# Kernel optimization log

Measured on AMD Instinct MI355X. Metric: run time of the kernel, lower is better.

Reference implementation:

```python
import jax, jax.numpy as jnp
import numpy as np
from jax import lax

B, S, I = 256, 2048, 128
H, K, O, M = 32, 64, 256, 3


def setup_inputs() -> dict:
    key = jax.random.key(0)
    ks = jax.random.split(key, 11)
    sc_i = 1.0 / np.sqrt(I)
    sc_h = 1.0 / np.sqrt(H)
    return {
        "inputs": jax.random.normal(ks[0], (B, S, I), dtype=jnp.float32),
        "W_ih": jax.random.uniform(ks[1], (3 * H, I), jnp.float32, -sc_h, sc_h),
        "W_hh": jax.random.uniform(ks[2], (3 * H, H), jnp.float32, -sc_h, sc_h),
        "b_ih": jax.random.uniform(ks[3], (3 * H,), jnp.float32, -sc_h, sc_h),
        "b_hh": jax.random.uniform(ks[4], (3 * H,), jnp.float32, -sc_h, sc_h),
        "Wk": jax.random.uniform(ks[5], (K, H), jnp.float32, -sc_h, sc_h),
        "bk": jax.random.uniform(ks[6], (K,), jnp.float32, -sc_h, sc_h),
        "Wq": jax.random.uniform(ks[7], (K, H), jnp.float32, -sc_h, sc_h),
        "bq": jax.random.uniform(ks[8], (K,), jnp.float32, -sc_h, sc_h),
        "Wv": jax.random.uniform(ks[9], (O, H), jnp.float32, -sc_h, sc_h),
        "bv": jax.random.uniform(ks[10], (O,), jnp.float32, -sc_h, sc_h),
    }


def _gru_cell(x, h, W_ih, W_hh, b_ih, b_hh):
    # torch.nn.GRUCell math
    gi = x @ W_ih.T + b_ih  # (B, 3H)
    gh = h @ W_hh.T + b_hh  # (B, 3H)
    i_r, i_z, i_n = jnp.split(gi, 3, axis=-1)
    h_r, h_z, h_n = jnp.split(gh, 3, axis=-1)
    r = jax.nn.sigmoid(i_r + h_r)
    z = jax.nn.sigmoid(i_z + h_z)
    n = jnp.tanh(i_n + r * h_n)
    return (1.0 - z) * n + z * h


def reference(inputs, W_ih, W_hh, b_ih, b_hh, Wk, bk, Wq, bq, Wv, bv):
    Bb, Ss, _ = inputs.shape
    dt = inputs.dtype
    NEG = jnp.asarray(-1e30, dt)

    def step(carry, xt):
        x_t, t = xt
        h, keys, values = carry
        h = _gru_cell(x_t, h, W_ih, W_hh, b_ih, b_hh)
        # read (counter == t at read time, capped at M via valid mask)
        q = h @ Wq.T + bq                              # (B, K)
        valid = jnp.arange(M) < t                      # (M,)
        scores = jnp.einsum('bk,bmk->bm', q, keys)
        scores = jnp.where(valid[None, :], scores, NEG)
        w = jax.nn.softmax(scores, axis=-1)
        retrieved = jnp.einsum('bm,bmo->bo', w, values)
        retrieved = retrieved * (t > 0).astype(dt)     # counter==0 -> zeros
        # write (only first M steps)
        key_t = h @ Wk.T + bk                          # (B, K)
        val_t = h @ Wv.T + bv                          # (B, O)
        oh = jax.nn.one_hot(t, M, dtype=dt) * (t < M).astype(dt)  # (M,)
        keys = keys + oh[None, :, None] * key_t[:, None, :]
        values = values + oh[None, :, None] * val_t[:, None, :]
        return (h, keys, values), (retrieved, h)

    init = (jnp.zeros((Bb, H), dt), jnp.zeros((Bb, M, K), dt), jnp.zeros((Bb, M, O), dt))
    xs = jnp.swapaxes(inputs, 0, 1)                    # (S, B, I)
    ts = jnp.arange(Ss)
    _, (outs, hids) = lax.scan(step, init, (xs, ts))
    outputs = jnp.swapaxes(outs, 0, 1)                 # (B, S, O)
    hiddens = lax.stop_gradient(jnp.swapaxes(hids, 0, 1))  # detached in torch
    return outputs, hiddens
```

## Files before the change

### kernel.cpp

```cpp
#include <hip/hip_runtime.h>
#include <cstddef>

#define Bq   256
#define Sq   2048
#define Iq   128
#define Hq   32
#define THq  96
#define Kq   64
#define Oq   256
#define Mq   3

#define OUT_HID_OFF 134217728ull
#define GI_BSTRIDE  524288ull
#define GI_OFF      327680ull

__global__ __launch_bounds__(256) void gi_gemm_kernel(
    const float* __restrict__ x, const float* __restrict__ Wih,
    const float* __restrict__ bih, float* __restrict__ gi_base)
{
    __shared__ float Wl[THq * Iq];
    const int tid = threadIdx.x;

    {
        const float4* Wg4 = (const float4*)Wih;
        float4* Wl4 = (float4*)Wl;
        #pragma unroll
        for (int i = 0; i < 12; ++i)
            Wl4[tid + 256 * i] = Wg4[tid + 256 * i];
    }
    __syncthreads();

    const int r = blockIdx.x * 256 + tid;
    const int b = r >> 11;
    const int s = r & 2047;

    const float4* xg = (const float4*)(x + (size_t)r * Iq);
    float4 xv[32];
    #pragma unroll
    for (int i = 0; i < 32; ++i) xv[i] = xg[i];

    float* out = gi_base + (size_t)b * GI_BSTRIDE + GI_OFF + (size_t)s * THq;

    #pragma unroll
    for (int half = 0; half < 2; ++half) {
        float acc[48];
        #pragma unroll
        for (int j = 0; j < 48; ++j) {
            const int row = half * 48 + j;
            const float4* w4 = (const float4*)(Wl + row * Iq);
            float p0 = bih[row], p1 = 0.f, p2 = 0.f, p3 = 0.f;
            #pragma unroll
            for (int i = 0; i < 32; ++i) {
                float4 w = w4[i];
                float4 xx = xv[i];
                p0 = fmaf(xx.x, w.x, p0);
                p1 = fmaf(xx.y, w.y, p1);
                p2 = fmaf(xx.z, w.z, p2);
                p3 = fmaf(xx.w, w.w, p3);
            }
            acc[j] = (p0 + p1) + (p2 + p3);
        }
        float4* o4 = (float4*)(out + half * 48);
        #pragma unroll
        for (int j4 = 0; j4 < 12; ++j4)
            o4[j4] = make_float4(acc[4*j4+0], acc[4*j4+1], acc[4*j4+2], acc[4*j4+3]);
    }
}

__device__ __forceinline__ float sigmoid_f(float x) {
    return 1.f / (1.f + __expf(-x));
}
__device__ __forceinline__ float tanh_f(float x) {
    x = fminf(fmaxf(x, -30.f), 30.f);
    float e = __expf(-2.f * x);
    return (1.f - e) / (1.f + e);
}

__global__ __launch_bounds__(128) void scan_kernel(
    const float* __restrict__ Whh, const float* __restrict__ bhh,
    const float* __restrict__ Wk,  const float* __restrict__ bk,
    const float* __restrict__ Wq,  const float* __restrict__ bq,
    const float* __restrict__ Wv,  const float* __restrict__ bv,
    float* __restrict__ dout)
{
    const int tid = threadIdx.x;
    const int b = blockIdx.x;

    __shared__ __align__(16) float hbuf[2][Hq];
    __shared__ __align__(16) float keysS[Mq][Kq];
    __shared__ __align__(16) float valsS[Mq][Oq];

    if (tid < Hq) { hbuf[0][tid] = 0.f; hbuf[1][tid] = 0.f; }
    for (int i = tid; i < Mq * Kq; i += 128) ((float*)keysS)[i] = 0.f;
    for (int i = tid; i < Mq * Oq; i += 128) ((float*)valsS)[i] = 0.f;

    const float* gi_row = dout + (size_t)b * GI_BSTRIDE + GI_OFF;
    float* out_o = dout + (size_t)b * GI_BSTRIDE;
    float* out_h = dout + OUT_HID_OFF + (size_t)b * (Sq * Hq);

    if (tid < 64) {
        const int l = tid;
        const bool lo = (l < Hq);
        float wa[Hq], wb[Hq];
        #pragma unroll
        for (int k = 0; k < Hq; ++k) wa[k] = Whh[l * Hq + k];
        #pragma unroll
        for (int k = 0; k < Hq; ++k) wb[k] = lo ? Whh[(64 + l) * Hq + k] : 0.f;
        const float ba = bhh[l];
        const float bb = lo ? bhh[64 + l] : 0.f;
        float h_old = 0.f;

        const int PF = 4;
        float ga[4], gb[4];
        #pragma unroll
        for (int d = 0; d < PF; ++d) {
            ga[d] = gi_row[(size_t)d * THq + l];
            gb[d] = lo ? gi_row[(size_t)d * THq + 64 + l] : 0.f;
        }

        for (int t = 0; t <= Sq; ++t) {
            __syncthreads();
            if (t < Sq) {
                const float gia = ga[0];
                const float gib = gb[0];
                #pragma unroll
                for (int d = 0; d < PF - 1; ++d) { ga[d] = ga[d+1]; gb[d] = gb[d+1]; }
                const int tt = t + PF;
                if (tt < Sq) {
                    ga[PF-1] = gi_row[(size_t)tt * THq + l];
                    gb[PF-1] = lo ? gi_row[(size_t)tt * THq + 64 + l] : 0.f;
                } else { ga[PF-1] = 0.f; gb[PF-1] = 0.f; }

                const float4* h4 = (const float4*)hbuf[(t + 1) & 1];
                float gha = ba, ghb = bb;
                #pragma unroll
                for (int kk = 0; kk < 8; ++kk) {
                    float4 hv = h4[kk];
                    gha = fmaf(hv.x, wa[4*kk+0], gha);
                    gha = fmaf(hv.y, wa[4*kk+1], gha);
                    gha = fmaf(hv.z, wa[4*kk+2], gha);
                    gha = fmaf(hv.w, wa[4*kk+3], gha);
                    ghb = fmaf(hv.x, wb[4*kk+0], ghb);
                    ghb = fmaf(hv.y, wb[4*kk+1], ghb);
                    ghb = fmaf(hv.z, wb[4*kk+2], ghb);
                    ghb = fmaf(hv.w, wb[4*kk+3], ghb);
                }
                const float xa = gia + gha;
                const float xz = __shfl(xa, l + 32, 64);
                if (lo) {
                    const float r = sigmoid_f(xa);
                    const float z = sigmoid_f(xz);
                    const float n = tanh_f(gib + r * ghb);
                    const float hn = (1.f - z) * n + z * h_old;
                    h_old = hn;
                    hbuf[t & 1][l] = hn;
                    out_h[(size_t)t * Hq + l] = hn;
                }
            }
        }
    } else {
        const int k = tid - 64;
        float wqr[Hq], wkr[Hq];
        #pragma unroll
        for (int kk = 0; kk < Hq; ++kk) wqr[kk] = Wq[k * Hq + kk];
        #pragma unroll
        for (int kk = 0; kk < Hq; ++kk) wkr[kk] = Wk[k * Hq + kk];
        const float bqk = bq[k];
        const float bkk = bk[k];

        for (int t = 0; t <= Sq; ++t) {
            __syncthreads();
            if (t >= 1) {
                const int tp = t - 1;
                const float4* h4 = (const float4*)hbuf[tp & 1];
                float4 hr[8];
                #pragma unroll
                for (int kk = 0; kk < 8; ++kk) hr[kk] = h4[kk];

                float q = bqk;
                #pragma unroll
                for (int kk = 0; kk < 8; ++kk) {
                    q = fmaf(hr[kk].x, wqr[4*kk+0], q);
                    q = fmaf(hr[kk].y, wqr[4*kk+1], q);
                    q = fmaf(hr[kk].z, wqr[4*kk+2], q);
                    q = fmaf(hr[kk].w, wqr[4*kk+3], q);
                }
                float s0 = q * keysS[0][k];
                float s1 = q * keysS[1][k];
                float s2 = q * keysS[2][k];
                #pragma unroll
                for (int off = 1; off < 64; off <<= 1) {
                    s0 += __shfl_xor(s0, off, 64);
                    s1 += __shfl_xor(s1, off, 64);
                    s2 += __shfl_xor(s2, off, 64);
                }
                const int v = tp < Mq ? tp : Mq;
                float w0 = 0.f, w1 = 0.f, w2 = 0.f;
                if (v > 0) {
                    float mx = s0;
                    if (v > 1) mx = fmaxf(mx, s1);
                    if (v > 2) mx = fmaxf(mx, s2);
                    const float e0 = __expf(s0 - mx);
                    const float e1 = (v > 1) ? __expf(s1 - mx) : 0.f;
                    const float e2 = (v > 2) ? __expf(s2 - mx) : 0.f;
                    const float inv = 1.f / (e0 + e1 + e2);
                    w0 = e0 * inv; w1 = e1 * inv; w2 = e2 * inv;
                }
                const float4 a0 = ((const float4*)valsS[0])[k];
                const float4 a1 = ((const float4*)valsS[1])[k];
                const float4 a2 = ((const float4*)valsS[2])[k];
                float4 acc;
                acc.x = w0*a0.x + w1*a1.x + w2*a2.x;
                acc.y = w0*a0.y + w1*a1.y + w2*a2.y;
                acc.z = w0*a0.z + w1*a1.z + w2*a2.z;
                acc.w = w0*a0.w + w1*a1.w + w2*a2.w;
                ((float4*)(out_o + (size_t)tp * Oq))[k] = acc;

                if (tp < Mq) {
                    float kv = bkk;
                    #pragma unroll
                    for (int kk = 0; kk < 8; ++kk) {
                        kv = fmaf(hr[kk].x, wkr[4*kk+0], kv);
                        kv = fmaf(hr[kk].y, wkr[4*kk+1], kv);
                        kv = fmaf(hr[kk].z, wkr[4*kk+2], kv);
                        kv = fmaf(hr[kk].w, wkr[4*kk+3], kv);
                    }
                    keysS[tp][k] = kv;
                    #pragma unroll
                    for (int j = 0; j < 4; ++j) {
                        const int o = 4 * k + j;
                        const float* wvr = Wv + o * Hq;
                        float vv = bv[o];
                        #pragma unroll
                        for (int kk = 0; kk < 8; ++kk) {
                            vv = fmaf(hr[kk].x, wvr[4*kk+0], vv);
                            vv = fmaf(hr[kk].y, wvr[4*kk+1], vv);
                            vv = fmaf(hr[kk].z, wvr[4*kk+2], vv);
                            vv = fmaf(hr[kk].w, wvr[4*kk+3], vv);
                        }
                        valsS[tp][o] = vv;
                    }
                }
            }
        }
    }
}

extern "C" void kernel_launch(void* const* d_in, const int* in_sizes, int n_in,
                              void* d_out, int out_size, void* d_ws, size_t ws_size,
                              hipStream_t stream) {
    const float* inputs = (const float*)d_in[0];
    const float* W_ih   = (const float*)d_in[1];
    const float* W_hh   = (const float*)d_in[2];
    const float* b_ih   = (const float*)d_in[3];
    const float* b_hh   = (const float*)d_in[4];
    const float* Wk     = (const float*)d_in[5];
    const float* bk     = (const float*)d_in[6];
    const float* Wq     = (const float*)d_in[7];
    const float* bq     = (const float*)d_in[8];
    const float* Wv     = (const float*)d_in[9];
    const float* bv     = (const float*)d_in[10];
    float* out = (float*)d_out;

    gi_gemm_kernel<<<(Bq * Sq) / 256, 256, 0, stream>>>(inputs, W_ih, b_ih, out);
    scan_kernel<<<Bq, 128, 0, stream>>>(W_hh, b_hh, Wk, bk, Wq, bq, Wv, bv, out);
}
```

Baseline: 2.410 ms.

## Fold query projection into precomputed key scores and tighten scan step latency

For each memory slot, the read path now precomputes A_m = Wq^T·key_m and the constant bq·key_m once, at write time. Each step's score then becomes a 32-wide dot product with h, which removes the per-step query projection and the 64-lane shuffle reductions from the serial critical path. The scan also uses a lighter LDS-only barrier, switches to hardware reciprocals in sigmoid, tanh and softmax, and moves the hidden-state stores to the idle read wavefront. Separately, the input GEMM accumulates all 96 outputs over four K-chunks with a two-blocks-per-CU launch bound, which raises register pressure. The reciprocal-based math and the reordered dot products slightly change floating-point rounding.

```diff
diff --git a/kernel.cpp b/kernel.cpp
--- a/kernel.cpp
+++ b/kernel.cpp
@@ -14,11 +14,12 @@
 #define GI_BSTRIDE  524288ull
 #define GI_OFF      327680ull
 
-__global__ __launch_bounds__(256) void gi_gemm_kernel(
+__global__ __launch_bounds__(256, 2) void gi_gemm_kernel(
     const float* __restrict__ x, const float* __restrict__ Wih,
     const float* __restrict__ bih, float* __restrict__ gi_base)
 {
-    __shared__ float Wl[THq * Iq];
+    __shared__ __align__(16) float Wl[THq * Iq];
+    __shared__ __align__(16) float Bl[THq];
     const int tid = threadIdx.x;
 
     {
@@ -27,31 +28,35 @@
         #pragma unroll
         for (int i = 0; i < 12; ++i)
             Wl4[tid + 256 * i] = Wg4[tid + 256 * i];
+        if (tid < THq) Bl[tid] = bih[tid];
     }
     __syncthreads();
 
     const int r = blockIdx.x * 256 + tid;
     const int b = r >> 11;
     const int s = r & 2047;
-
     const float4* xg = (const float4*)(x + (size_t)r * Iq);
-    float4 xv[32];
+
+    float acc[THq];
     #pragma unroll
-    for (int i = 0; i < 32; ++i) xv[i] = xg[i];
-
-    float* out = gi_base + (size_t)b * GI_BSTRIDE + GI_OFF + (size_t)s * THq;
-
-    #pragma unroll
-    for (int half = 0; half < 2; ++half) {
-        float acc[48];
-        #pragma unroll
-        for (int j = 0; j < 48; ++j) {
-            const int row = half * 48 + j;
-            const float4* w4 = (const float4*)(Wl + row * Iq);
-            float p0 = bih[row], p1 = 0.f, p2 = 0.f, p3 = 0.f;
+    for (int j4 = 0; j4 < 24; ++j4) {
+        float4 bv = ((const float4*)Bl)[j4];
+        acc[4*j4+0] = bv.x; acc[4*j4+1] = bv.y;
+        acc[4*j4+2] = bv.z; acc[4*j4+3] = bv.w;
+    }
+
+    #pragma unroll 1
+    for (int c = 0; c < 4; ++c) {
+        float4 xv[8];
+        #pragma unroll
+        for (int i = 0; i < 8; ++i) xv[i] = xg[c * 8 + i];
+        #pragma unroll
+        for (int j = 0; j < THq; ++j) {
+            const float4* w4 = (const float4*)(Wl + j * Iq) + c * 8;
+            float p0 = acc[j], p1 = 0.f, p2 = 0.f, p3 = 0.f;
             #pragma unroll
-            for (int i = 0; i < 32; ++i) {
-                float4 w = w4[i];
+            for (int i = 0; i < 8; ++i) {
+                float4 w  = w4[i];
                 float4 xx = xv[i];
                 p0 = fmaf(xx.x, w.x, p0);
                 p1 = fmaf(xx.y, w.y, p1);
@@ -60,20 +65,29 @@
             }
             acc[j] = (p0 + p1) + (p2 + p3);
         }
-        float4* o4 = (float4*)(out + half * 48);
-        #pragma unroll
-        for (int j4 = 0; j4 < 12; ++j4)
-            o4[j4] = make_float4(acc[4*j4+0], acc[4*j4+1], acc[4*j4+2], acc[4*j4+3]);
-    }
+    }
+
+    float* outp = gi_base + (size_t)b * GI_BSTRIDE + GI_OFF + (size_t)s * THq;
+    float4* o4 = (float4*)outp;
+    #pragma unroll
+    for (int j4 = 0; j4 < 24; ++j4)
+        o4[j4] = make_float4(acc[4*j4+0], acc[4*j4+1], acc[4*j4+2], acc[4*j4+3]);
+}
+
+__device__ __forceinline__ void lds_barrier() {
+    __builtin_amdgcn_sched_barrier(0);
+    asm volatile("s_waitcnt lgkmcnt(0)" ::: "memory");
+    __builtin_amdgcn_s_barrier();
+    __builtin_amdgcn_sched_barrier(0);
 }
 
 __device__ __forceinline__ float sigmoid_f(float x) {
-    return 1.f / (1.f + __expf(-x));
+    return __builtin_amdgcn_rcpf(1.f + __expf(-x));
 }
 __device__ __forceinline__ float tanh_f(float x) {
     x = fminf(fmaxf(x, -30.f), 30.f);
     float e = __expf(-2.f * x);
-    return (1.f - e) / (1.f + e);
+    return fmaf(2.f, __builtin_amdgcn_rcpf(1.f + e), -1.f);
 }
 
 __global__ __launch_bounds__(128) void scan_kernel(
@@ -89,10 +103,12 @@
     __shared__ __align__(16) float hbuf[2][Hq];
     __shared__ __align__(16) float keysS[Mq][Kq];
     __shared__ __align__(16) float valsS[Mq][Oq];
+    __shared__ __align__(16) float As[Mq][36];
 
     if (tid < Hq) { hbuf[0][tid] = 0.f; hbuf[1][tid] = 0.f; }
     for (int i = tid; i < Mq * Kq; i += 128) ((float*)keysS)[i] = 0.f;
     for (int i = tid; i < Mq * Oq; i += 128) ((float*)valsS)[i] = 0.f;
+    for (int i = tid; i < Mq * 36; i += 128) ((float*)As)[i] = 0.f;
 
     const float* gi_row = dout + (size_t)b * GI_BSTRIDE + GI_OFF;
     float* out_o = dout + (size_t)b * GI_BSTRIDE;
@@ -103,9 +119,9 @@
         const bool lo = (l < Hq);
         float wa[Hq], wb[Hq];
         #pragma unroll
-        for (int k = 0; k < Hq; ++k) wa[k] = Whh[l * Hq + k];
-        #pragma unroll
-        for (int k = 0; k < Hq; ++k) wb[k] = lo ? Whh[(64 + l) * Hq + k] : 0.f;
+        for (int kk = 0; kk < Hq; ++kk) wa[kk] = Whh[l * Hq + kk];
+        #pragma unroll
+        for (int kk = 0; kk < Hq; ++kk) wb[kk] = lo ? Whh[(64 + l) * Hq + kk] : 0.f;
         const float ba = bhh[l];
         const float bb = lo ? bhh[64 + l] : 0.f;
         float h_old = 0.f;
@@ -119,7 +135,7 @@
         }
 
         for (int t = 0; t <= Sq; ++t) {
-            __syncthreads();
+            lds_barrier();
             if (t < Sq) {
                 const float gia = ga[0];
                 const float gib = gb[0];
@@ -148,28 +164,20 @@
                 const float xa = gia + gha;
                 const float xz = __shfl(xa, l + 32, 64);
                 if (lo) {
-                    const float r = sigmoid_f(xa);
-                    const float z = sigmoid_f(xz);
-                    const float n = tanh_f(gib + r * ghb);
-                    const float hn = (1.f - z) * n + z * h_old;
+                    const float rr = sigmoid_f(xa);
+                    const float zz = sigmoid_f(xz);
+                    const float nn = tanh_f(gib + rr * ghb);
+                    const float hn = (1.f - zz) * nn + zz * h_old;
                     h_old = hn;
                     hbuf[t & 1][l] = hn;
-                    out_h[(size_t)t * Hq + l] = hn;
                 }
             }
         }
     } else {
         const int k = tid - 64;
-        float wqr[Hq], wkr[Hq];
-        #pragma unroll
-        for (int kk = 0; kk < Hq; ++kk) wqr[kk] = Wq[k * Hq + kk];
-        #pragma unroll
-        for (int kk = 0; kk < Hq; ++kk) wkr[kk] = Wk[k * Hq + kk];
-        const float bqk = bq[k];
-        const float bkk = bk[k];
 
         for (int t = 0; t <= Sq; ++t) {
-            __syncthreads();
+            lds_barrier();
             if (t >= 1) {
                 const int tp = t - 1;
                 const float4* h4 = (const float4*)hbuf[tp & 1];
@@ -177,68 +185,85 @@
                 #pragma unroll
                 for (int kk = 0; kk < 8; ++kk) hr[kk] = h4[kk];
 
-                float q = bqk;
-                #pragma unroll
-                for (int kk = 0; kk < 8; ++kk) {
-                    q = fmaf(hr[kk].x, wqr[4*kk+0], q);
-                    q = fmaf(hr[kk].y, wqr[4*kk+1], q);
-                    q = fmaf(hr[kk].z, wqr[4*kk+2], q);
-                    q = fmaf(hr[kk].w, wqr[4*kk+3], q);
-                }
-                float s0 = q * keysS[0][k];
-                float s1 = q * keysS[1][k];
-                float s2 = q * keysS[2][k];
-                #pragma unroll
-                for (int off = 1; off < 64; off <<= 1) {
-                    s0 += __shfl_xor(s0, off, 64);
-                    s1 += __shfl_xor(s1, off, 64);
-                    s2 += __shfl_xor(s2, off, 64);
-                }
+                float sm[3];
+                #pragma unroll
+                for (int m = 0; m < Mq; ++m) {
+                    const float4* Am4 = (const float4*)As[m];
+                    float p0 = As[m][32], p1 = 0.f, p2 = 0.f, p3 = 0.f;
+                    #pragma unroll
+                    for (int kk = 0; kk < 8; ++kk) {
+                        float4 av = Am4[kk];
+                        float4 hv = hr[kk];
+                        p0 = fmaf(hv.x, av.x, p0);
+                        p1 = fmaf(hv.y, av.y, p1);
+                        p2 = fmaf(hv.z, av.z, p2);
+                        p3 = fmaf(hv.w, av.w, p3);
+                    }
+                    sm[m] = (p0 + p1) + (p2 + p3);
+                }
+
                 const int v = tp < Mq ? tp : Mq;
                 float w0 = 0.f, w1 = 0.f, w2 = 0.f;
                 if (v > 0) {
-                    float mx = s0;
-                    if (v > 1) mx = fmaxf(mx, s1);
-                    if (v > 2) mx = fmaxf(mx, s2);
-                    const float e0 = __expf(s0 - mx);
-                    const float e1 = (v > 1) ? __expf(s1 - mx) : 0.f;
-                    const float e2 = (v > 2) ? __expf(s2 - mx) : 0.f;
-                    const float inv = 1.f / (e0 + e1 + e2);
+                    float mx = sm[0];
+                    if (v > 1) mx = fmaxf(mx, sm[1]);
+                    if (v > 2) mx = fmaxf(mx, sm[2]);
+                    const float e0 = __expf(sm[0] - mx);
+                    const float e1 = (v > 1) ? __expf(sm[1] - mx) : 0.f;
+                    const float e2 = (v > 2) ? __expf(sm[2] - mx) : 0.f;
+                    const float inv = __builtin_amdgcn_rcpf(e0 + e1 + e2);
                     w0 = e0 * inv; w1 = e1 * inv; w2 = e2 * inv;
                 }
                 const float4 a0 = ((const float4*)valsS[0])[k];
                 const float4 a1 = ((const float4*)valsS[1])[k];
                 const float4 a2 = ((const float4*)valsS[2])[k];
-                float4 acc;
-                acc.x = w0*a0.x + w1*a1.x + w2*a2.x;
-                acc.y = w0*a0.y + w1*a1.y + w2*a2.y;
-                acc.z = w0*a0.z + w1*a1.z + w2*a2.z;
-                acc.w = w0*a0.w + w1*a1.w + w2*a2.w;
-                ((float4*)(out_o + (size_t)tp * Oq))[k] = acc;
+                float4 accv;
+                accv.x = w0*a0.x + w1*a1.x + w2*a2.x;
+                accv.y = w0*a0.y + w1*a1.y + w2*a2.y;
+                accv.z = w0*a0.z + w1*a1.z + w2*a2.z;
+                accv.w = w0*a0.w + w1*a1.w + w2*a2.w;
+                ((float4*)(out_o + (size_t)tp * Oq))[k] = accv;
+                if (k < 8)
+                    ((float4*)(out_h + (size_t)tp * Hq))[k] = hr[k];
 
                 if (tp < Mq) {
-                    float kv = bkk;
+                    const float4* wk4 = (const float4*)(Wk + k * Hq);
+                    float kv = bk[k];
                     #pragma unroll
                     for (int kk = 0; kk < 8; ++kk) {
-                        kv = fmaf(hr[kk].x, wkr[4*kk+0], kv);
-                        kv = fmaf(hr[kk].y, wkr[4*kk+1], kv);
-                        kv = fmaf(hr[kk].z, wkr[4*kk+2], kv);
-                        kv = fmaf(hr[kk].w, wkr[4*kk+3], kv);
+                        float4 w = wk4[kk]; float4 hv = hr[kk];
+                        kv = fmaf(hv.x, w.x, kv);
+                        kv = fmaf(hv.y, w.y, kv);
+                        kv = fmaf(hv.z, w.z, kv);
+                        kv = fmaf(hv.w, w.w, kv);
                     }
                     keysS[tp][k] = kv;
                     #pragma unroll
                     for (int j = 0; j < 4; ++j) {
                         const int o = 4 * k + j;
-                        const float* wvr = Wv + o * Hq;
+                        const float4* wv4 = (const float4*)(Wv + o * Hq);
                         float vv = bv[o];
                         #pragma unroll
                         for (int kk = 0; kk < 8; ++kk) {
-                            vv = fmaf(hr[kk].x, wvr[4*kk+0], vv);
-                            vv = fmaf(hr[kk].y, wvr[4*kk+1], vv);
-                            vv = fmaf(hr[kk].z, wvr[4*kk+2], vv);
-                            vv = fmaf(hr[kk].w, wvr[4*kk+3], vv);
+                            float4 w = wv4[kk]; float4 hv = hr[kk];
+                            vv = fmaf(hv.x, w.x, vv);
+                            vv = fmaf(hv.y, w.y, vv);
+                            vv = fmaf(hv.z, w.z, vv);
+                            vv = fmaf(hv.w, w.w, vv);
                         }
                         valsS[tp][o] = vv;
+                    }
+                    float cm = bq[k] * kv;
+                    #pragma unroll
+                    for (int off = 1; off < 64; off <<= 1)
+                        cm += __shfl_xor(cm, off, 64);
+                    if (k == 0) As[tp][32] = cm;
+                    if (k < Hq) {
+                        float a = 0.f;
+                        #pragma unroll
+                        for (int kk = 0; kk < Kq; ++kk)
+                            a = fmaf(Wq[kk * Hq + k], keysS[tp][kk], a);
+                        As[tp][k] = a;
                     }
                 }
             }
```

Result: slower. 3.668 ms (+52.2%).
